# Kernel optimization log

Hardware: AMD Instinct MI355X
Metric: run time of the kernel (lower is better)

Reference implementation:

```python
import jax, jax.numpy as jnp
import numpy as np

B, SEQ, C, H = 4, 1024, 256, 4
Dk = C // H                                  # 64
L = 4 * SEQ                                  # 4096 attention length
FACTOR = 4
N_TOP = FACTOR * int(np.ceil(np.log(L)))     # U = 36 dominant queries
SAMPLE_K = FACTOR * int(np.ceil(np.log(L)))  # u = 36 sampled keys per query


def _forward(et, mp, co, vol, Wq, bq, Wk, bk, Wv, bv, Wo, bo, index_sample):
    sz = et.shape[0]
    # student_graph input shuffle (faithful to the torch .view calls)
    x = jnp.concatenate([et.reshape(SEQ, -1), co.reshape(SEQ, -1),
                         mp.reshape(SEQ, -1), vol.reshape(SEQ, -1)], axis=-1)
    x = x.reshape(sz, L, C)  # [B, 4*seq_len, d_model]
    # projections; ProbAttention uses view(B,H,L,-1) which is a raw reshape
    # (NOT a transpose) of the [B,L,H,Dk] tensor -> fuse into one reshape
    q = (x @ Wq + bq).reshape(sz, H, L, Dk)
    k = (x @ Wk + bk).reshape(sz, H, L, Dk)
    v = (x @ Wv + bv).reshape(sz, H, L, Dk)
    # _prob_QK: random key sampling + sparsity measure + top-k query select
    K_sample = k[:, :, index_sample, :]                        # [B,H,L,u,Dk]
    QKs = jnp.einsum('bhse,bhske->bhsk', q, K_sample)          # [B,H,L,u]
    M = QKs.max(axis=-1) - QKs.sum(axis=-1) / L                # [B,H,L]
    _, m_top = jax.lax.top_k(M, N_TOP)                         # [B,H,U]
    q_red = jnp.take_along_axis(q, m_top[..., None], axis=2)   # [B,H,U,Dk]
    scores = jnp.einsum('bhue,bhle->bhul', q_red, k) * (1.0 / float(np.sqrt(Dk)))
    attn = jax.nn.softmax(scores, axis=-1)                     # [B,H,U,L]
    upd = jnp.einsum('bhul,bhld->bhud', attn, v)               # [B,H,U,Dk]
    # initial context = V-sum broadcast; scatter dense update at top queries
    ctx = jnp.broadcast_to(v.sum(axis=2, keepdims=True), (sz, H, L, Dk))
    bi = jnp.arange(sz)[:, None, None]
    hi = jnp.arange(H)[None, :, None]
    ctx = ctx.at[bi, hi, m_top, :].set(upd)                    # [B,H,L,Dk]
    # AttentionLayer output: .view(B, L, -1) on contiguous [B,H,L,Dk] is again
    # a raw reshape (faithful), then out projection
    out = ctx.reshape(sz, L, H * Dk) @ Wo + bo                 # [B,L,C]
    return out.reshape(SEQ, -1)


def setup_inputs():
    key = jax.random.key(0)
    ks = jax.random.split(key, 13)
    f = lambda i, shp: jax.random.normal(ks[i], shp, jnp.float32)
    ws = 1.0 / float(np.sqrt(C))  # keep logits in a sane range
    return {
        'et': f(0, (B, SEQ, C)), 'mp': f(1, (B, SEQ, C)),
        'co': f(2, (B, SEQ, C)), 'vol': f(3, (B, SEQ, C)),
        'Wq': f(4, (C, C)) * ws, 'bq': f(5, (C,)) * 0.01,
        'Wk': f(6, (C, C)) * ws, 'bk': f(7, (C,)) * 0.01,
        'Wv': f(8, (C, C)) * ws, 'bv': f(9, (C,)) * 0.01,
        'Wo': f(10, (C, C)) * ws, 'bo': f(11, (C,)) * 0.01,
        'index_sample': jax.random.randint(ks[12], (L, SAMPLE_K), 0, L, dtype=jnp.int32),
        'comp_idx': 0,
    }


def reference(et, mp, co, vol, Wq, bq, Wk, bk, Wv, bv, Wo, bo, index_sample, comp_idx):
    return _forward(et, mp, co, vol, Wq, bq, Wk, bk, Wv, bv, Wo, bo, index_sample)
```

## Files before the change

kernel.cpp:

```cpp
#include <hip/hip_runtime.h>
#include <hip/hip_bf16.h>

#define BHn 16
#define Ln 4096
#define NTOP 36
#define SKn 36
#define NCHUNK 64

using s16x8 = __attribute__((ext_vector_type(8))) short;
using u16x8 = __attribute__((ext_vector_type(8))) unsigned short;
using f32x4 = __attribute__((ext_vector_type(4))) float;

__device__ __forceinline__ unsigned short bf_hi(float f) {
  unsigned u = __float_as_uint(f);
  return (unsigned short)((u + 0x7fffu + ((u >> 16) & 1u)) >> 16);
}

__global__ __launch_bounds__(256) void wxconv(
    const float* __restrict__ W0, const float* __restrict__ W1, const float* __restrict__ W2,
    unsigned short* __restrict__ th0, unsigned short* __restrict__ tl0,
    unsigned short* __restrict__ th1, unsigned short* __restrict__ tl1,
    unsigned short* __restrict__ th2, unsigned short* __restrict__ tl2,
    const float* __restrict__ s0, const float* __restrict__ s1,
    const float* __restrict__ s2, const float* __restrict__ s3,
    unsigned short* __restrict__ Axh, unsigned short* __restrict__ Axl) {
  int bx = blockIdx.x;
  int t = threadIdx.x;
  if (bx < 48) {
    int wsel = bx >> 4;
    const float* W = (wsel == 0) ? W0 : (wsel == 1) ? W1 : W2;
    unsigned short* TH = (wsel == 0) ? th0 : (wsel == 1) ? th1 : th2;
    unsigned short* TL = (wsel == 0) ? tl0 : (wsel == 1) ? tl1 : tl2;
    int kr = (bx & 15) * 16;
    int n = t;
    u16x8 hv[2], lv[2];
#pragma unroll
    for (int j = 0; j < 16; ++j) {
      float f = W[(size_t)(kr + j) * 256 + n];
      unsigned short h = bf_hi(f);
      float lof = f - __uint_as_float(((unsigned)h) << 16);
      hv[j >> 3][j & 7] = h;
      lv[j >> 3][j & 7] = bf_hi(lof);
    }
    *(u16x8*)&TH[(size_t)n * 256 + kr] = hv[0];
    *(u16x8*)&TH[(size_t)n * 256 + kr + 8] = hv[1];
    *(u16x8*)&TL[(size_t)n * 256 + kr] = lv[0];
    *(u16x8*)&TL[(size_t)n * 256 + kr + 8] = lv[1];
  } else {
    int row = (bx - 48) * 4 + (t >> 6);
    int c = t & 63;
    int l = row & 4095, b = row >> 12;
    int part = (l >> 2) & 3;
    int seq = ((l >> 4) << 2) | (l & 3);
    const float* sp = (part == 0) ? s0 : (part == 1) ? s1 : (part == 2) ? s2 : s3;
    float4 f = ((const float4*)(sp + (size_t)((b << 10) + seq) * 256))[c];
    float fv[4] = {f.x, f.y, f.z, f.w};
    ushort4 hv, lv;
    unsigned short* hp = (unsigned short*)&hv;
    unsigned short* lp = (unsigned short*)&lv;
#pragma unroll
    for (int j = 0; j < 4; ++j) {
      unsigned short h = bf_hi(fv[j]);
      float lof = fv[j] - __uint_as_float(((unsigned)h) << 16);
      hp[j] = h;
      lp[j] = bf_hi(lof);
    }
    *(ushort4*)&Axh[(size_t)row * 256 + c * 4] = hv;
    *(ushort4*)&Axl[(size_t)row * 256 + c * 4] = lv;
  }
}

#define LDW 40
__global__ __launch_bounds__(256, 3) void qkv_mfma(
    const unsigned short* __restrict__ Axh, const unsigned short* __restrict__ Axl,
    const unsigned short* __restrict__ th0, const unsigned short* __restrict__ tl0,
    const unsigned short* __restrict__ th1, const unsigned short* __restrict__ tl1,
    const unsigned short* __restrict__ th2, const unsigned short* __restrict__ tl2,
    const float* __restrict__ b0, const float* __restrict__ b1, const float* __restrict__ b2,
    float* __restrict__ o0, float* __restrict__ o1, float* __restrict__ o2) {
  __shared__ __align__(16) unsigned short Ah[128 * LDW];
  __shared__ __align__(16) unsigned short Al[128 * LDW];
  __shared__ __align__(16) unsigned short Bh[128 * LDW];
  __shared__ __align__(16) unsigned short Bl[128 * LDW];
  int t = threadIdx.x;
  int g = blockIdx.x;
  int vnt = g >> 7;
  int wsel = vnt >> 1;
  int col0 = (vnt & 1) * 128;
  int row0 = (g & 127) * 128;
  const unsigned short* TH = (wsel == 0) ? th0 : (wsel == 1) ? th1 : th2;
  const unsigned short* TL = (wsel == 0) ? tl0 : (wsel == 1) ? tl1 : tl2;
  const float* bias = (wsel == 0) ? b0 : (wsel == 1) ? b1 : b2;
  float* O = (wsel == 0) ? o0 : (wsel == 1) ? o1 : o2;
  const bool vlite = (wsel == 2);

  int srow = t >> 1, half = t & 1;
  const unsigned short* ah_g = Axh + (size_t)(row0 + srow) * 256 + half * 16;
  const unsigned short* al_g = Axl + (size_t)(row0 + srow) * 256 + half * 16;
  const unsigned short* bh_g = TH + (size_t)(col0 + srow) * 256 + half * 16;
  const unsigned short* bl_g = TL + (size_t)(col0 + srow) * 256 + half * 16;

  int lane = t & 63;
  int wv = t >> 6;
  int wr = wv >> 1, wc = wv & 1;
  int fr = lane & 15, fk = lane >> 4;
  int aoff = (wr * 64 + fr) * LDW + fk * 8;
  int boff = (wc * 64 + fr) * LDW + fk * 8;

  f32x4 acc[4][4] = {};

  for (int k0 = 0; k0 < 256; k0 += 32) {
    int wa = srow * LDW + half * 16;
    u16x8 va0 = *(const u16x8*)(ah_g + k0);
    u16x8 va1 = *(const u16x8*)(ah_g + k0 + 8);
    u16x8 vb0 = *(const u16x8*)(bh_g + k0);
    u16x8 vb1 = *(const u16x8*)(bh_g + k0 + 8);
    *(u16x8*)&Ah[wa] = va0; *(u16x8*)&Ah[wa + 8] = va1;
    *(u16x8*)&Bh[wa] = vb0; *(u16x8*)&Bh[wa + 8] = vb1;
    if (!vlite) {
      u16x8 vl0 = *(const u16x8*)(al_g + k0);
      u16x8 vl1 = *(const u16x8*)(al_g + k0 + 8);
      u16x8 vc0 = *(const u16x8*)(bl_g + k0);
      u16x8 vc1 = *(const u16x8*)(bl_g + k0 + 8);
      *(u16x8*)&Al[wa] = vl0; *(u16x8*)&Al[wa + 8] = vl1;
      *(u16x8*)&Bl[wa] = vc0; *(u16x8*)&Bl[wa + 8] = vc1;
    }
    __syncthreads();

    if (vlite) {
      s16x8 fah[4];
#pragma unroll
      for (int mi = 0; mi < 4; ++mi)
        fah[mi] = *(const s16x8*)&Ah[aoff + mi * 16 * LDW];
#pragma unroll
      for (int ni = 0; ni < 4; ++ni) {
        s16x8 fbh = *(const s16x8*)&Bh[boff + ni * 16 * LDW];
#pragma unroll
        for (int mi = 0; mi < 4; ++mi)
          acc[mi][ni] = __builtin_amdgcn_mfma_f32_16x16x32_bf16(fah[mi], fbh, acc[mi][ni], 0, 0, 0);
      }
    } else {
      s16x8 fah[4], fal[4];
#pragma unroll
      for (int mi = 0; mi < 4; ++mi) {
        fah[mi] = *(const s16x8*)&Ah[aoff + mi * 16 * LDW];
        fal[mi] = *(const s16x8*)&Al[aoff + mi * 16 * LDW];
      }
#pragma unroll
      for (int ni = 0; ni < 4; ++ni) {
        s16x8 fbh = *(const s16x8*)&Bh[boff + ni * 16 * LDW];
        s16x8 fbl = *(const s16x8*)&Bl[boff + ni * 16 * LDW];
#pragma unroll
        for (int mi = 0; mi < 4; ++mi) {
          acc[mi][ni] = __builtin_amdgcn_mfma_f32_16x16x32_bf16(fah[mi], fbh, acc[mi][ni], 0, 0, 0);
          acc[mi][ni] = __builtin_amdgcn_mfma_f32_16x16x32_bf16(fal[mi], fbh, acc[mi][ni], 0, 0, 0);
          acc[mi][ni] = __builtin_amdgcn_mfma_f32_16x16x32_bf16(fah[mi], fbl, acc[mi][ni], 0, 0, 0);
        }
      }
    }
    __syncthreads();
  }

#pragma unroll
  for (int ni = 0; ni < 4; ++ni) {
    int n = col0 + wc * 64 + ni * 16 + fr;
    float bv = bias[n];
#pragma unroll
    for (int mi = 0; mi < 4; ++mi) {
      int mb = row0 + wr * 64 + mi * 16 + fk * 4;
#pragma unroll
      for (int r = 0; r < 4; ++r)
        O[(size_t)(mb + r) * 256 + n] = acc[mi][ni][r] + bv;
    }
  }
}

__global__ __launch_bounds__(256) void qks_m3(
    const float* __restrict__ q, const float* __restrict__ k,
    const int* __restrict__ idxs, float* __restrict__ Mout) {
  __shared__ float qs[64][68];
  __shared__ int il[64 * SKn];
  int g = blockIdx.x;
  int x = g & 7;
  int i = g >> 3;
  int bh = (x << 1) | (i >> 6);
  int s0 = (i & 63) * 64;
  int t = threadIdx.x;
  size_t base = (size_t)bh << 12;
  for (int i2 = t; i2 < 1024; i2 += 256) {
    int row = i2 >> 4, d4 = i2 & 15;
    *(float4*)&qs[row][d4 * 4] = ((const float4*)(q + (base + s0 + row) * 64))[d4];
  }
  for (int i2 = t; i2 < 64 * SKn; i2 += 256) il[i2] = idxs[s0 * SKn + i2];
  __syncthreads();
  int sl = t >> 2;
  int dq = t & 3;
  float qr[16];
#pragma unroll
  for (int i2 = 0; i2 < 4; ++i2)
    *(float4*)&qr[i2 * 4] = *(const float4*)&qs[sl][i2 * 16 + dq * 4];
  float mx = -INFINITY, sm = 0.f;
  const float4* kb4 = (const float4*)(k + base * 64);
#pragma unroll 4
  for (int j = 0; j < SKn; ++j) {
    int l = il[sl * SKn + j];
    const float4* kr = kb4 + (size_t)l * 16;
    float acc = 0.f;
#pragma unroll
    for (int i2 = 0; i2 < 4; ++i2) {
      float4 kv = kr[i2 * 4 + dq];
      acc += kv.x * qr[i2 * 4] + kv.y * qr[i2 * 4 + 1] + kv.z * qr[i2 * 4 + 2] + kv.w * qr[i2 * 4 + 3];
    }
    acc += __shfl_xor(acc, 1, 64);
    acc += __shfl_xor(acc, 2, 64);
    mx = fmaxf(mx, acc);
    sm += acc;
  }
  if (dq == 0) Mout[base + s0 + sl] = mx - sm * (1.0f / 4096.0f);
}

__global__ __launch_bounds__(256) void topk_radix(
    const float* __restrict__ M, int* __restrict__ topidx) {
  __shared__ unsigned hist[4096];
  __shared__ unsigned sup[256];
  __shared__ unsigned cand_u[256];
  __shared__ int cand_i[256];
  __shared__ int s_bin1, s_bin2, s_above, s_ocnt, s_ccnt;
  int bh = blockIdx.x;
  int t = threadIdx.x;
  int mbase = bh * 4096;
  unsigned uv[16];
  for (int i = t; i < 4096; i += 256) hist[i] = 0;
  __syncthreads();
#pragma unroll
  for (int r = 0; r < 16; ++r) {
    unsigned b = __float_as_uint(M[mbase + t + 256 * r]);
    unsigned u = b ^ ((unsigned)((int)b >> 31) | 0x80000000u);
    uv[r] = u;
    atomicAdd(&hist[u >> 20], 1u);
  }
  __syncthreads();
  {
    unsigned ssum = 0;
    for (int i = 0; i < 16; ++i) ssum += hist[t * 16 + i];
    sup[t] = ssum;
  }
  __syncthreads();
  if (t == 0) {
    unsigned cum = 0; int sb = 255;
    for (; sb > 0; --sb) { if (cum + sup[sb] >= NTOP) break; cum += sup[sb]; }
    int b = sb * 16 + 15;
    for (; b > sb * 16; --b) { if (cum + hist[b] >= NTOP) break; cum += hist[b]; }
    s_bin1 = b; s_above = (int)cum;
  }
  __syncthreads();
  int bin1 = s_bin1;
  int need1 = NTOP - s_above;
  __syncthreads();
  for (int i = t; i < 4096; i += 256) hist[i] = 0;
  __syncthreads();
#pragma unroll
  for (int r = 0; r < 16; ++r)
    if ((int)(uv[r] >> 20) == bin1) atomicAdd(&hist[(uv[r] >> 8) & 0xFFF], 1u);
  __syncthreads();
  {
    unsigned ssum = 0;
    for (int i = 0; i < 16; ++i) ssum += hist[t * 16 + i];
    sup[t] = ssum;
  }
  __syncthreads();
  if (t == 0) {
    unsigned cum = 0; int sb = 255;
    for (; sb > 0; --sb) { if (cum + sup[sb] >= (unsigned)need1) break; cum += sup[sb]; }
    int b = sb * 16 + 15;
    for (; b > sb * 16; --b) { if (cum + hist[b] >= (unsigned)need1) break; cum += hist[b]; }
    s_bin2 = b; s_above += (int)cum;
    s_ocnt = 0; s_ccnt = 0;
  }
  __syncthreads();
  int bin2 = s_bin2;
  int need = NTOP - s_above;
  int* outp = topidx + bh * NTOP;
#pragma unroll
  for (int r = 0; r < 16; ++r) {
    unsigned u = uv[r];
    int b1 = u >> 20, b2 = (u >> 8) & 0xFFF;
    if (b1 > bin1 || (b1 == bin1 && b2 > bin2)) {
      int p = atomicAdd(&s_ocnt, 1);
      outp[p] = t + 256 * r;
    } else if (b1 == bin1 && b2 == bin2) {
      int p = atomicAdd(&s_ccnt, 1);
      if (p < 256) { cand_u[p] = u; cand_i[p] = t + 256 * r; }
    }
  }
  __syncthreads();
  if (t == 0) {
    int cc = s_ccnt < 256 ? s_ccnt : 256;
    int slot = s_ocnt;
    for (int n = 0; n < need; ++n) {
      unsigned bu = 0; int bi = 0x7fffffff, bp = -1;
      for (int c = 0; c < cc; ++c) {
        if (cand_i[c] < 0) continue;
        if (cand_u[c] > bu || (cand_u[c] == bu && cand_i[c] < bi)) {
          bu = cand_u[c]; bi = cand_i[c]; bp = c;
        }
      }
      outp[slot++] = bi;
      cand_i[bp] = -1;
    }
  }
}

__global__ __launch_bounds__(256) void attn_partial(
    const float* __restrict__ q, const float* __restrict__ k,
    const float* __restrict__ v, const int* __restrict__ topidx,
    float* __restrict__ part_m, float* __restrict__ part_s,
    float* __restrict__ part_o, float* __restrict__ vpart2) {
  __shared__ float4 Ks4[64][17];
  __shared__ float4 qs4[36][17];
  __shared__ float S[36][68];
  int g = blockIdx.x;
  int x = g & 7;
  int i = g >> 3;
  int bh = (x << 1) | (i >> 6);
  int c = i & 63;
  int l0 = c * 64;
  int t = threadIdx.x;
  size_t base = (size_t)bh * 4096;

  const float4* kg = (const float4*)(k + (base + l0) * 64);
  for (int i2 = t; i2 < 64 * 16; i2 += 256) {
    int row = i2 >> 4, d4 = i2 & 15;
    Ks4[row][d4] = kg[row * 16 + d4];
  }
  for (int i2 = t; i2 < 36 * 16; i2 += 256) {
    int u = i2 >> 4, d4 = i2 & 15;
    int m = topidx[bh * NTOP + u];
    qs4[u][d4] = ((const float4*)(q + (base + m) * 64))[d4];
  }
  __syncthreads();

  {
    int l = t & 63, ug = t >> 6;
    float acc[9] = {};
#pragma unroll
    for (int d4 = 0; d4 < 16; ++d4) {
      float4 kv = Ks4[l][d4];
#pragma unroll
      for (int j = 0; j < 9; ++j) {
        float4 qv = qs4[ug * 9 + j][d4];
        acc[j] += kv.x * qv.x + kv.y * qv.y + kv.z * qv.z + kv.w * qv.w;
      }
    }
#pragma unroll
    for (int j = 0; j < 9; ++j) S[ug * 9 + j][l] = acc[j] * 0.125f;
  }
  __syncthreads();

  if (t < NTOP) {
    float mx = -INFINITY;
    for (int l = 0; l < 64; ++l) mx = fmaxf(mx, S[t][l]);
    float sm = 0.f;
    for (int l = 0; l < 64; ++l) { float e = expf(S[t][l] - mx); S[t][l] = e; sm += e; }
    part_m[((size_t)bh * NCHUNK + c) * NTOP + t] = mx;
    part_s[((size_t)bh * NCHUNK + c) * NTOP + t] = sm;
  }
  __syncthreads();

  {
    int d = t & 63, ug = t >> 6;
    float pacc[9] = {};
    float vs = 0.f;
    const float* vg = v + (base + l0) * 64;
    for (int l = 0; l < 64; ++l) {
      float vv = vg[l * 64 + d];
      vs += vv;
#pragma unroll
      for (int j = 0; j < 9; ++j) pacc[j] += S[ug * 9 + j][l] * vv;
    }
#pragma unroll
    for (int j = 0; j < 9; ++j)
      part_o[(((size_t)bh * NCHUNK + c) * NTOP + ug * 9 + j) * 64 + d] = pacc[j];
    if (ug == 0) vpart2[((size_t)bh * NCHUNK + c) * 64 + d] = vs;
  }
}

__global__ __launch_bounds__(256) void attn_combine(
    const float* __restrict__ part_m, const float* __restrict__ part_s,
    const float* __restrict__ part_o, float* __restrict__ upd) {
  __shared__ float wl[4][64];
  int wave = threadIdx.x >> 6;
  int lane = threadIdx.x & 63;
  int widx = blockIdx.x * 4 + wave;
  int bh = widx / NTOP;
  int u = widx % NTOP;
  float m_c = part_m[((size_t)bh * NCHUNK + lane) * NTOP + u];
  float M = m_c;
#pragma unroll
  for (int off = 32; off > 0; off >>= 1) M = fmaxf(M, __shfl_xor(M, off, 64));
  float w = expf(m_c - M);
  float ds = part_s[((size_t)bh * NCHUNK + lane) * NTOP + u] * w;
#pragma unroll
  for (int off = 32; off > 0; off >>= 1) ds += __shfl_xor(ds, off, 64);
  wl[wave][lane] = w;
  __syncthreads();
  float acc = 0.f;
  for (int c2 = 0; c2 < NCHUNK; ++c2)
    acc += part_o[(((size_t)bh * NCHUNK + c2) * NTOP + u) * 64 + lane] * wl[wave][c2];
  upd[(size_t)widx * 64 + lane] = acc / ds;
}

__global__ __launch_bounds__(256) void vsum_out(
    const float* __restrict__ vpart2, const float* __restrict__ Wo,
    const float* __restrict__ bo, float* __restrict__ vsum,
    float* __restrict__ outbase) {
  __shared__ float red[4][64];
  __shared__ float vs[64];
  int bh = blockIdx.x;
  int t = threadIdx.x;
  int d = t & 63, qq = t >> 6;
  float acc = 0.f;
  for (int c = qq; c < NCHUNK; c += 4)
    acc += vpart2[((size_t)bh * NCHUNK + c) * 64 + d];
  red[qq][d] = acc;
  __syncthreads();
  if (qq == 0) {
    float s = red[0][d] + red[1][d] + red[2][d] + red[3][d];
    vs[d] = s;
    vsum[bh * 64 + d] = s;
  }
  __syncthreads();
  float ob = bo[t];
#pragma unroll 8
  for (int dd = 0; dd < 64; ++dd) {
    float w4 = Wo[dd * 256 + t] + Wo[(64 + dd) * 256 + t] +
               Wo[(128 + dd) * 256 + t] + Wo[(192 + dd) * 256 + t];
    ob += vs[dd] * w4;
  }
  outbase[bh * 256 + t] = ob;
}

__global__ __launch_bounds__(256) void out_fill(
    const float* __restrict__ outbase, float4* __restrict__ out4) {
  int g = blockIdx.x * 256 + threadIdx.x;
  int c4 = g & 63;
  int bh = g >> 16;
  out4[g] = ((const float4*)outbase)[bh * 64 + c4];
}

__global__ __launch_bounds__(256) void out_patch(
    const float* __restrict__ upd, const float* __restrict__ vsum,
    const int* __restrict__ topidx, const float* __restrict__ Wo,
    float* __restrict__ out) {
  __shared__ float dv[64];
  int bhu = blockIdx.x;
  int bh = bhu / NTOP;
  int h = bh & 3, b = bh >> 2;
  int t = threadIdx.x;
  if (t < 64) dv[t] = upd[(size_t)bhu * 64 + t] - vsum[bh * 64 + t];
  __syncthreads();
  int m = topidx[bhu];
  int j = m & 3;
  int lp = h * 1024 + (m >> 2);
  float acc = 0.f;
#pragma unroll 8
  for (int d = 0; d < 64; ++d) acc += dv[d] * Wo[(j * 64 + d) * 256 + t];
  atomicAdd(&out[((size_t)(b * 4096 + lp)) * 256 + t], acc);
}

extern "C" void kernel_launch(void* const* d_in, const int* in_sizes, int n_in,
                              void* d_out, int out_size, void* d_ws, size_t ws_size,
                              hipStream_t stream) {
  const float* et  = (const float*)d_in[0];
  const float* mp  = (const float*)d_in[1];
  const float* co  = (const float*)d_in[2];
  const float* vol = (const float*)d_in[3];
  const float* Wq = (const float*)d_in[4];
  const float* bq = (const float*)d_in[5];
  const float* Wk = (const float*)d_in[6];
  const float* bk = (const float*)d_in[7];
  const float* Wv = (const float*)d_in[8];
  const float* bv = (const float*)d_in[9];
  const float* Wo = (const float*)d_in[10];
  const float* bo = (const float*)d_in[11];
  const int* idxs = (const int*)d_in[12];
  float* out = (float*)d_out;

  char* ws = (char*)d_ws;
  const size_t BIG = 16u * 1024u * 1024u;
  float* qb = (float*)(ws);
  float* kb = (float*)(ws + BIG);
  float* vb = (float*)(ws + 2 * BIG);
  char* sm = ws + 3 * BIG;
  float* Mbuf   = (float*)(sm);
  int*   topidx = (int*)(sm + 262144);
  float* vsum   = (float*)(sm + 262144 + 4096);
  char* pm = sm + 262144 + 4096 + 8192;
  float* part_m = (float*)(pm);
  float* part_s = (float*)(pm + 147456);
  float* part_o = (float*)(pm + 2 * 147456);
  float* updb   = (float*)(pm + 2 * 147456 + 9437184);
  float* outbase = (float*)(pm + 2 * 147456 + 9437184 + 147456);
  unsigned short* wt = (unsigned short*)(pm + 2 * 147456 + 9437184 + 147456 + 16384);
  unsigned short* wth0 = wt;
  unsigned short* wtl0 = wt + 65536;
  unsigned short* wth1 = wt + 2 * 65536;
  unsigned short* wtl1 = wt + 3 * 65536;
  unsigned short* wth2 = wt + 4 * 65536;
  unsigned short* wtl2 = wt + 5 * 65536;
  unsigned short* axh = wt + 6 * 65536;
  unsigned short* axl = axh + 16384 * 256;
  float* vpart2 = (float*)(axl + 16384 * 256);

  wxconv<<<4144, 256, 0, stream>>>(Wq, Wk, Wv, wth0, wtl0, wth1, wtl1, wth2, wtl2,
                                   et, co, mp, vol, axh, axl);

  qkv_mfma<<<768, 256, 0, stream>>>(
      axh, axl, wth0, wtl0, wth1, wtl1, wth2, wtl2, bq, bk, bv, qb, kb, vb);

  qks_m3<<<1024, 256, 0, stream>>>(qb, kb, idxs, Mbuf);

  topk_radix<<<BHn, 256, 0, stream>>>(Mbuf, topidx);

  attn_partial<<<1024, 256, 0, stream>>>(
      qb, kb, vb, topidx, part_m, part_s, part_o, vpart2);
  attn_combine<<<144, 256, 0, stream>>>(part_m, part_s, part_o, updb);

  vsum_out<<<BHn, 256, 0, stream>>>(vpart2, Wo, bo, vsum, outbase);

  out_fill<<<4096, 256, 0, stream>>>(outbase, (float4*)out);
  out_patch<<<BHn * NTOP, 256, 0, stream>>>(updb, vsum, topidx, Wo, out);
}
```

Baseline: 141.1 us.

## Fuse attention combine into output patch, store partials in bf16, parallelize softmax

Merges the separate combine kernel into the output-patch kernel, removing one launch and the intermediate upd buffer. Partial attention outputs are stored as bf16, halving the partial write and read traffic, at some precision cost. The per-chunk softmax is now split across 4 threads per query with shuffle reductions, replacing a single serial thread per query. The combine also uses a full 256-thread block per query.

After: 127.4 us. 1.11x faster.

```diff
diff --git a/kernel.cpp b/kernel.cpp
--- a/kernel.cpp
+++ b/kernel.cpp
@@ -315,7 +315,7 @@
     const float* __restrict__ q, const float* __restrict__ k,
     const float* __restrict__ v, const int* __restrict__ topidx,
     float* __restrict__ part_m, float* __restrict__ part_s,
-    float* __restrict__ part_o, float* __restrict__ vpart2) {
+    unsigned short* __restrict__ part_ob, float* __restrict__ vpart2) {
   __shared__ float4 Ks4[64][17];
   __shared__ float4 qs4[36][17];
   __shared__ float S[36][68];
@@ -357,13 +357,27 @@
   }
   __syncthreads();
 
-  if (t < NTOP) {
+  if (t < 144) {
+    int u = t >> 2, p = t & 3;
+    int lb = p * 16;
     float mx = -INFINITY;
-    for (int l = 0; l < 64; ++l) mx = fmaxf(mx, S[t][l]);
+#pragma unroll
+    for (int l2 = 0; l2 < 16; ++l2) mx = fmaxf(mx, S[u][lb + l2]);
+    mx = fmaxf(mx, __shfl_xor(mx, 1, 64));
+    mx = fmaxf(mx, __shfl_xor(mx, 2, 64));
     float sm = 0.f;
-    for (int l = 0; l < 64; ++l) { float e = expf(S[t][l] - mx); S[t][l] = e; sm += e; }
-    part_m[((size_t)bh * NCHUNK + c) * NTOP + t] = mx;
-    part_s[((size_t)bh * NCHUNK + c) * NTOP + t] = sm;
+#pragma unroll
+    for (int l2 = 0; l2 < 16; ++l2) {
+      float e = expf(S[u][lb + l2] - mx);
+      S[u][lb + l2] = e;
+      sm += e;
+    }
+    sm += __shfl_xor(sm, 1, 64);
+    sm += __shfl_xor(sm, 2, 64);
+    if (p == 0) {
+      part_m[((size_t)bh * NCHUNK + c) * NTOP + u] = mx;
+      part_s[((size_t)bh * NCHUNK + c) * NTOP + u] = sm;
+    }
   }
   __syncthreads();
 
@@ -380,34 +394,9 @@
     }
 #pragma unroll
     for (int j = 0; j < 9; ++j)
-      part_o[(((size_t)bh * NCHUNK + c) * NTOP + ug * 9 + j) * 64 + d] = pacc[j];
+      part_ob[(((size_t)bh * NCHUNK + c) * NTOP + ug * 9 + j) * 64 + d] = bf_hi(pacc[j]);
     if (ug == 0) vpart2[((size_t)bh * NCHUNK + c) * 64 + d] = vs;
   }
-}
-
-__global__ __launch_bounds__(256) void attn_combine(
-    const float* __restrict__ part_m, const float* __restrict__ part_s,
-    const float* __restrict__ part_o, float* __restrict__ upd) {
-  __shared__ float wl[4][64];
-  int wave = threadIdx.x >> 6;
-  int lane = threadIdx.x & 63;
-  int widx = blockIdx.x * 4 + wave;
-  int bh = widx / NTOP;
-  int u = widx % NTOP;
-  float m_c = part_m[((size_t)bh * NCHUNK + lane) * NTOP + u];
-  float M = m_c;
-#pragma unroll
-  for (int off = 32; off > 0; off >>= 1) M = fmaxf(M, __shfl_xor(M, off, 64));
-  float w = expf(m_c - M);
-  float ds = part_s[((size_t)bh * NCHUNK + lane) * NTOP + u] * w;
-#pragma unroll
-  for (int off = 32; off > 0; off >>= 1) ds += __shfl_xor(ds, off, 64);
-  wl[wave][lane] = w;
-  __syncthreads();
-  float acc = 0.f;
-  for (int c2 = 0; c2 < NCHUNK; ++c2)
-    acc += part_o[(((size_t)bh * NCHUNK + c2) * NTOP + u) * 64 + lane] * wl[wave][c2];
-  upd[(size_t)widx * 64 + lane] = acc / ds;
 }
 
 __global__ __launch_bounds__(256) void vsum_out(
@@ -448,24 +437,54 @@
   out4[g] = ((const float4*)outbase)[bh * 64 + c4];
 }
 
-__global__ __launch_bounds__(256) void out_patch(
-    const float* __restrict__ upd, const float* __restrict__ vsum,
+__global__ __launch_bounds__(256) void combine_patch(
+    const float* __restrict__ part_m, const float* __restrict__ part_s,
+    const unsigned short* __restrict__ part_ob, const float* __restrict__ vsum,
     const int* __restrict__ topidx, const float* __restrict__ Wo,
     float* __restrict__ out) {
+  __shared__ float wl[64];
+  __shared__ float red[4][64];
   __shared__ float dv[64];
-  int bhu = blockIdx.x;
-  int bh = bhu / NTOP;
+  __shared__ float ds_s;
+  int widx = blockIdx.x;
+  int bh = widx / NTOP;
+  int u = widx % NTOP;
+  int t = threadIdx.x;
+  int d = t & 63, qq = t >> 6;
+  if (t < 64) {
+    float m_c = part_m[((size_t)bh * NCHUNK + t) * NTOP + u];
+    float M = m_c;
+#pragma unroll
+    for (int off = 32; off > 0; off >>= 1) M = fmaxf(M, __shfl_xor(M, off, 64));
+    float w = expf(m_c - M);
+    float ds = part_s[((size_t)bh * NCHUNK + t) * NTOP + u] * w;
+#pragma unroll
+    for (int off = 32; off > 0; off >>= 1) ds += __shfl_xor(ds, off, 64);
+    wl[t] = w;
+    if (t == 0) ds_s = ds;
+  }
+  __syncthreads();
+  float acc = 0.f;
+#pragma unroll
+  for (int j = 0; j < 16; ++j) {
+    int c = qq + j * 4;
+    float po = __uint_as_float(
+        ((unsigned)part_ob[(((size_t)bh * NCHUNK + c) * NTOP + u) * 64 + d]) << 16);
+    acc += po * wl[c];
+  }
+  red[qq][d] = acc;
+  __syncthreads();
+  if (qq == 0)
+    dv[d] = (red[0][d] + red[1][d] + red[2][d] + red[3][d]) / ds_s - vsum[bh * 64 + d];
+  __syncthreads();
+  int m = topidx[widx];
   int h = bh & 3, b = bh >> 2;
-  int t = threadIdx.x;
-  if (t < 64) dv[t] = upd[(size_t)bhu * 64 + t] - vsum[bh * 64 + t];
-  __syncthreads();
-  int m = topidx[bhu];
-  int j = m & 3;
+  int j2 = m & 3;
   int lp = h * 1024 + (m >> 2);
-  float acc = 0.f;
+  float acc2 = 0.f;
 #pragma unroll 8
-  for (int d = 0; d < 64; ++d) acc += dv[d] * Wo[(j * 64 + d) * 256 + t];
-  atomicAdd(&out[((size_t)(b * 4096 + lp)) * 256 + t], acc);
+  for (int dd = 0; dd < 64; ++dd) acc2 += dv[dd] * Wo[(j2 * 64 + dd) * 256 + t];
+  atomicAdd(&out[((size_t)(b * 4096 + lp)) * 256 + t], acc2);
 }
 
 extern "C" void kernel_launch(void* const* d_in, const int* in_sizes, int n_in,
@@ -498,10 +517,9 @@
   char* pm = sm + 262144 + 4096 + 8192;
   float* part_m = (float*)(pm);
   float* part_s = (float*)(pm + 147456);
-  float* part_o = (float*)(pm + 2 * 147456);
-  float* updb   = (float*)(pm + 2 * 147456 + 9437184);
-  float* outbase = (float*)(pm + 2 * 147456 + 9437184 + 147456);
-  unsigned short* wt = (unsigned short*)(pm + 2 * 147456 + 9437184 + 147456 + 16384);
+  unsigned short* part_ob = (unsigned short*)(pm + 2 * 147456);
+  float* outbase = (float*)(pm + 2 * 147456 + 4718592);
+  unsigned short* wt = (unsigned short*)(pm + 2 * 147456 + 4718592 + 16384);
   unsigned short* wth0 = wt;
   unsigned short* wtl0 = wt + 65536;
   unsigned short* wth1 = wt + 2 * 65536;
@@ -523,11 +541,12 @@
   topk_radix<<<BHn, 256, 0, stream>>>(Mbuf, topidx);
 
   attn_partial<<<1024, 256, 0, stream>>>(
-      qb, kb, vb, topidx, part_m, part_s, part_o, vpart2);
-  attn_combine<<<144, 256, 0, stream>>>(part_m, part_s, part_o, updb);
+      qb, kb, vb, topidx, part_m, part_s, part_ob, vpart2);
 
   vsum_out<<<BHn, 256, 0, stream>>>(vpart2, Wo, bo, vsum, outbase);
 
   out_fill<<<4096, 256, 0, stream>>>(outbase, (float4*)out);
-  out_patch<<<BHn * NTOP, 256, 0, stream>>>(updb, vsum, topidx, Wo, out);
-}
+
+  combine_patch<<<BHn * NTOP, 256, 0, stream>>>(
+      part_m, part_s, part_ob, vsum, topidx, Wo, out);
+}
```
